# Kernel optimization log

Hardware: AMD Instinct MI355X
Metric: run time of the kernel (lower is better)

Reference implementation:

```python
import jax, jax.numpy as jnp
import numpy as np

B, N, C = 4, 100000, 64
S = 256            # img_size
RADIUS_PX = 1.5    # radius in pixels
K = 8              # points_per_pixel
GAMMA = 1.0
R_NDC = RADIUS_PX / S * 2.0  # radius in NDC, as in forward()


def setup_inputs() -> dict:
    key = jax.random.key(0)
    k1, k2 = jax.random.split(key)
    pts = jax.random.normal(k1, (B, N, 3), dtype=jnp.float32)
    features = jax.random.normal(k2, (B, N, C), dtype=jnp.float32)
    return {"pts": pts, "features": features}


def _rasterize_one(pts_b):
    # pts_b: (N,3) sign-flipped NDC points. Emulates pytorch3d rasterize_points:
    # per pixel keep the K nearest-in-z points whose NDC distance to the pixel
    # center is <= R_NDC (points with z < 0 are culled).
    x, y, z = pts_b[:, 0], pts_b[:, 1], pts_b[:, 2]
    # pytorch3d NDC->pixel: ndc = 1 - 2*(p+0.5)/S  =>  p = (1-ndc)*S/2 - 0.5
    px = (1.0 - x) * (S / 2.0) - 0.5
    py = (1.0 - y) * (S / 2.0) - 0.5
    offs = jnp.arange(-1, 3)  # 4-wide window fully covers a 1.5px radius
    cj = jnp.floor(px).astype(jnp.int32)[:, None] + offs  # (N,4) candidate cols
    ci = jnp.floor(py).astype(jnp.int32)[:, None] + offs  # (N,4) candidate rows
    cx = 1.0 - 2.0 * (cj.astype(pts_b.dtype) + 0.5) / S   # pixel-center NDC x
    cy = 1.0 - 2.0 * (ci.astype(pts_b.dtype) + 0.5) / S   # pixel-center NDC y
    d2 = (cy - y[:, None])[:, :, None] ** 2 + (cx - x[:, None])[:, None, :] ** 2  # (N,4,4)
    pid = ci[:, :, None] * S + cj[:, None, :]                                      # (N,4,4)
    inb = (ci[:, :, None] >= 0) & (ci[:, :, None] < S) & (cj[:, None, :] >= 0) & (cj[:, None, :] < S)
    valid = inb & (d2 <= R_NDC * R_NDC) & (z[:, None, None] >= 0.0)
    pid = jnp.where(valid, pid, S * S).reshape(-1)
    zc = jnp.where(valid, z[:, None, None], jnp.inf).reshape(-1)
    d2f = d2.reshape(-1)
    pidx = jnp.broadcast_to(jnp.arange(N, dtype=jnp.int32)[:, None, None], (N, 4, 4)).reshape(-1)
    order = jnp.lexsort((zc, pid))  # sort by pixel id, then depth (front first)
    pid_s, d2_s, pi_s = pid[order], d2f[order], pidx[order]
    seg_start = jnp.searchsorted(pid_s, pid_s, side='left')
    rank = jnp.arange(pid_s.shape[0]) - seg_start  # per-pixel z-rank
    keep = (pid_s < S * S) & (rank < K)
    pid_w = jnp.where(keep, pid_s, S * S)          # OOB index -> dropped by mode='drop'
    rank_w = jnp.where(keep, rank, 0)
    idx_buf = jnp.full((S * S, K), -1, jnp.int32).at[pid_w, rank_w].set(pi_s, mode='drop')
    d_buf = jnp.zeros((S * S, K), pts_b.dtype).at[pid_w, rank_w].set(d2_s, mode='drop')
    return idx_buf.reshape(S, S, K), d_buf.reshape(S, S, K)


def _forward(pts, features):
    # forward() flips x and y signs in-place
    pts = pts * jnp.array([-1.0, -1.0, 1.0], dtype=pts.dtype)
    idx, d2 = jax.vmap(_rasterize_one)(pts)        # (B,S,S,K) each
    dist = d2 / (R_NDC * R_NDC)
    alphas = 1.0 - jnp.clip(dist, 0.001, 1.0) ** (0.5 * GAMMA)  # .pow(0.5).pow(gamma)
    alphas = jnp.where(idx >= 0, alphas, 0.0)      # alpha_composite skips idx < 0
    trans = jnp.cumprod(1.0 - alphas, axis=-1)     # transmittance, front-to-back
    trans = jnp.concatenate([jnp.ones_like(trans[..., :1]), trans[..., :-1]], axis=-1)
    w = alphas * trans                             # (B,S,S,K) compositing weights
    gath = jax.vmap(lambda f, i: f[jnp.clip(i, 0)])(features, idx)  # (B,S,S,K,C)
    return jnp.einsum('bhwk,bhwkc->bchw', w, gath)  # (B,C,S,S)


def reference(pts, features):
    return _forward(pts, features)
```

## Files before the change

### kernel.cpp

```cpp
#include <hip/hip_runtime.h>
#include <stdint.h>

#pragma clang fp contract(off)

#define S 256
#define NPTS 100000
#define BATCH 4
#define CCH 64
#define K 8
#define CAP 20

static constexpr float R2 = 0.01171875f * 0.01171875f;
static constexpr unsigned long long SENT = 0xFFFFFFFFFFFFFFFFULL;

__global__ __launch_bounds__(256) void scatter_list_kernel(
        const float* __restrict__ pts,
        unsigned int* __restrict__ counts,
        unsigned long long* __restrict__ lists) {
    int gid = blockIdx.x * blockDim.x + threadIdx.x;
    if (gid >= BATCH * NPTS * 16) return;
    int cell = gid & 15;
    int pid  = gid >> 4;
    int b = pid / NPTS;
    int n = pid - b * NPTS;

    const float* p = pts + (size_t)pid * 3;
    float x = -p[0];
    float y = -p[1];
    float z = p[2];
    if (!(z >= 0.0f)) return;

    float px = (1.0f - x) * 128.0f - 0.5f;
    float py = (1.0f - y) * 128.0f - 0.5f;
    int cj0 = (int)floorf(px);
    int ci0 = (int)floorf(py);

    int ci = ci0 - 1 + (cell >> 2);
    int cj = cj0 - 1 + (cell & 3);
    if (ci < 0 || ci >= S || cj < 0 || cj >= S) return;

    float cy = 1.0f - 2.0f * ((float)ci + 0.5f) / 256.0f;
    float cx = 1.0f - 2.0f * ((float)cj + 0.5f) / 256.0f;
    float dy = cy - y;
    float dx = cx - x;
    float d2 = dy * dy + dx * dx;
    if (!(d2 <= R2)) return;

    unsigned long long key =
        ((unsigned long long)__float_as_uint(z) << 32) | (unsigned int)n;
    size_t base = (size_t)b * (S * S) + (size_t)(ci * S + cj);
    unsigned int old = atomicAdd(&counts[base], 1u);
    if (old < CAP) lists[base * CAP + old] = key;
}

#define CSW(a, b) do {                                        \
        unsigned long long _lo = (a) < (b) ? (a) : (b);       \
        unsigned long long _hi = (a) < (b) ? (b) : (a);       \
        (a) = _lo; (b) = _hi;                                 \
    } while (0)
#define INSERT8(x) do {                                       \
        unsigned long long _x = (x);                          \
        t7 = t7 < _x ? t7 : _x;                               \
        CSW(t6, t7); CSW(t5, t6); CSW(t4, t5); CSW(t3, t4);   \
        CSW(t2, t3); CSW(t1, t2); CSW(t0, t1);                \
    } while (0)
#define PAIR(j, q) do {                                                   \
        INSERT8((2 * (j)     < c) ? (q).x : SENT);                        \
        INSERT8((2 * (j) + 1 < c) ? (q).y : SENT);                        \
    } while (0)

__global__ __launch_bounds__(256) void blend_list_kernel(
        const float* __restrict__ pts,
        const float* __restrict__ feat,
        const unsigned int* __restrict__ counts,
        const unsigned long long* __restrict__ lists,
        float* __restrict__ out) {
    int blk = blockIdx.x;
    int logical = (blk & 7) * 512 + (blk >> 3);
    int seg = logical & 3;
    int h   = (logical >> 2) & 255;
    int b   = logical >> 10;
    int tid = threadIdx.x;
    int w0  = seg * 64;

    __shared__ float s_alpha[64][K + 1];
    __shared__ float s_wgt[64][K + 1];
    __shared__ int   s_idx[64][K + 1];
    __shared__ int   s_cnt[64];
    __shared__ unsigned long long s_key[64][K + 1];

    const float* pb = pts + (size_t)b * NPTS * 3;

    if (tid < 64) {
        size_t base = (size_t)b * (S * S) + (size_t)h * S + (size_t)(w0 + tid);
        const ulonglong2* lp2 =
            reinterpret_cast<const ulonglong2*>(lists + base * (size_t)CAP);

        ulonglong2 q0 = lp2[0], q1 = lp2[1], q2 = lp2[2], q3 = lp2[3];
        ulonglong2 q4 = lp2[4], q5 = lp2[5], q6 = lp2[6], q7 = lp2[7];
        ulonglong2 q8 = lp2[8], q9 = lp2[9];
        int c = (int)counts[base];
        if (c > CAP) c = CAP;

        unsigned long long t0 = SENT, t1 = SENT, t2 = SENT, t3 = SENT;
        unsigned long long t4 = SENT, t5 = SENT, t6 = SENT, t7 = SENT;

        PAIR(0, q0); PAIR(1, q1); PAIR(2, q2); PAIR(3, q3); PAIR(4, q4);
        PAIR(5, q5); PAIR(6, q6); PAIR(7, q7); PAIR(8, q8); PAIR(9, q9);

        s_key[tid][0] = t0; s_key[tid][1] = t1;
        s_key[tid][2] = t2; s_key[tid][3] = t3;
        s_key[tid][4] = t4; s_key[tid][5] = t5;
        s_key[tid][6] = t6; s_key[tid][7] = t7;
        s_cnt[tid] = c < K ? c : K;
    }
    __syncthreads();

    for (int e = tid; e < 64 * K; e += 256) {
        int p = e >> 3;
        int k = e & 7;
        unsigned long long key = s_key[p][k];
        float alpha = 0.0f;
        int idx = 0;
        if (key != SENT) {
            idx = (int)(unsigned int)(key & 0xFFFFFFFFULL);
            float x = -pb[(size_t)idx * 3 + 0];
            float y = -pb[(size_t)idx * 3 + 1];
            int w = w0 + p;
            float cy = 1.0f - 2.0f * ((float)h + 0.5f) / 256.0f;
            float cx = 1.0f - 2.0f * ((float)w + 0.5f) / 256.0f;
            float dy = cy - y;
            float dx = cx - x;
            float d2 = dy * dy + dx * dx;
            float dist = d2 / R2;
            dist = fminf(fmaxf(dist, 0.001f), 1.0f);
            alpha = 1.0f - sqrtf(dist);
        }
        s_alpha[p][k] = alpha;
        s_idx[p][k] = idx;
    }
    __syncthreads();

    if (tid < 64) {
        float t = 1.0f;
#pragma unroll
        for (int k = 0; k < K; ++k) {
            float a = s_alpha[tid][k];
            s_wgt[tid][k] = a * t;
            t *= (1.0f - a);
        }
    }
    __syncthreads();

    int wave = tid >> 6;
    int lane = tid & 63;
    int pbase = wave * 16;

    int kmax = 0;
#pragma unroll
    for (int i = 0; i < 16; ++i) {
        int c = s_cnt[pbase + i];
        kmax = c > kmax ? c : kmax;
    }

    float acc[16];
#pragma unroll
    for (int i = 0; i < 16; ++i) acc[i] = 0.0f;

    const float* fbl = feat + (size_t)b * NPTS * CCH + lane;
#pragma unroll 2
    for (int k = 0; k < kmax; ++k) {
        float v[16];
#pragma unroll
        for (int i = 0; i < 16; ++i) {
            int idx = s_idx[pbase + i][k];
            v[i] = fbl[(size_t)idx << 6];
        }
#pragma unroll
        for (int i = 0; i < 16; ++i) {
            acc[i] += s_wgt[pbase + i][k] * v[i];
        }
    }

    size_t obase = (((size_t)b * CCH + lane) * S + h) * S + (size_t)(w0 + pbase);
    float4* o4 = (float4*)(out + obase);
#pragma unroll
    for (int q = 0; q < 4; ++q) {
        o4[q] = make_float4(acc[4 * q + 0], acc[4 * q + 1],
                            acc[4 * q + 2], acc[4 * q + 3]);
    }
}

__global__ __launch_bounds__(256) void scatter_kernel(
        const float* __restrict__ pts,
        unsigned long long* __restrict__ keys) {
    int gid = blockIdx.x * blockDim.x + threadIdx.x;
    if (gid >= BATCH * NPTS * 16) return;
    int cell = gid & 15;
    int pid  = gid >> 4;
    int b = pid / NPTS;
    int n = pid - b * NPTS;

    const float* p = pts + (size_t)pid * 3;
    float x = -p[0];
    float y = -p[1];
    float z = p[2];
    if (!(z >= 0.0f)) return;

    float px = (1.0f - x) * 128.0f - 0.5f;
    float py = (1.0f - y) * 128.0f - 0.5f;
    int cj0 = (int)floorf(px);
    int ci0 = (int)floorf(py);

    int ci = ci0 - 1 + (cell >> 2);
    int cj = cj0 - 1 + (cell & 3);
    if (ci < 0 || ci >= S || cj < 0 || cj >= S) return;

    float cy = 1.0f - 2.0f * ((float)ci + 0.5f) / 256.0f;
    float cx = 1.0f - 2.0f * ((float)cj + 0.5f) / 256.0f;
    float dy = cy - y;
    float dx = cx - x;
    float d2 = dy * dy + dx * dx;
    if (!(d2 <= R2)) return;

    unsigned long long key =
        ((unsigned long long)__float_as_uint(z) << 32) | (unsigned int)n;
    unsigned long long* slot =
        keys + ((size_t)b * S * S + (size_t)(ci * S + cj)) * K;

    if (slot[K - 1] < key) return;

    for (int s = 0; s < K; ++s) {
        if (key == SENT) break;
        unsigned long long old = atomicMin(&slot[s], key);
        key = old > key ? old : key;
    }
}

__global__ __launch_bounds__(256) void blend_kernel(
        const float* __restrict__ pts,
        const float* __restrict__ feat,
        const unsigned long long* __restrict__ keys,
        float* __restrict__ out) {
    int seg = blockIdx.x;
    int h   = blockIdx.y;
    int b   = blockIdx.z;
    int tid = threadIdx.x;
    int w0  = seg * 64;

    __shared__ float s_alpha[64][K + 1];
    __shared__ float s_wgt[64][K + 1];
    __shared__ int   s_idx[64][K + 1];
    __shared__ int   s_cnt[64];

    const unsigned long long* kb =
        keys + ((size_t)b * S * S + (size_t)h * S + w0) * K;
    const float* pb = pts + (size_t)b * NPTS * 3;

    for (int e = tid; e < 64 * K; e += 256) {
        int p = e >> 3;
        int k = e & 7;
        unsigned long long key = kb[(size_t)p * K + k];
        float alpha = 0.0f;
        int idx = -1;
        if (key != SENT) {
            idx = (int)(unsigned int)(key & 0xFFFFFFFFULL);
            float x = -pb[(size_t)idx * 3 + 0];
            float y = -pb[(size_t)idx * 3 + 1];
            int w = w0 + p;
            float cy = 1.0f - 2.0f * ((float)h + 0.5f) / 256.0f;
            float cx = 1.0f - 2.0f * ((float)w + 0.5f) / 256.0f;
            float dy = cy - y;
            float dx = cx - x;
            float d2 = dy * dy + dx * dx;
            float dist = d2 / R2;
            dist = fminf(fmaxf(dist, 0.001f), 1.0f);
            alpha = 1.0f - sqrtf(dist);
        }
        s_alpha[p][k] = alpha;
        s_idx[p][k] = idx;
    }
    __syncthreads();

    if (tid < 64) {
        float t = 1.0f;
        int cnt = 0;
        for (int k = 0; k < K; ++k) {
            int raw = s_idx[tid][k];
            float a = s_alpha[tid][k];
            s_wgt[tid][k] = a * t;
            t *= (1.0f - a);
            if (raw >= 0) cnt = k + 1;
            s_idx[tid][k] = raw < 0 ? 0 : raw;
        }
        s_cnt[tid] = cnt;
    }
    __syncthreads();

    int wave = tid >> 6;
    int lane = tid & 63;
    int pbase = wave * 16;

    int kmax = 0;
#pragma unroll
    for (int i = 0; i < 16; ++i) {
        int c = s_cnt[pbase + i];
        kmax = c > kmax ? c : kmax;
    }

    float acc[16];
#pragma unroll
    for (int i = 0; i < 16; ++i) acc[i] = 0.0f;

    const float* fbl = feat + (size_t)b * NPTS * CCH + lane;
    for (int k = 0; k < kmax; ++k) {
        float v[16];
#pragma unroll
        for (int i = 0; i < 16; ++i) {
            int idx = s_idx[pbase + i][k];
            v[i] = fbl[(size_t)idx << 6];
        }
#pragma unroll
        for (int i = 0; i < 16; ++i) {
            acc[i] += s_wgt[pbase + i][k] * v[i];
        }
    }

    size_t obase = (((size_t)b * CCH + lane) * S + h) * S + (size_t)(w0 + pbase);
    float4* o4 = (float4*)(out + obase);
#pragma unroll
    for (int q = 0; q < 4; ++q) {
        o4[q] = make_float4(acc[4 * q + 0], acc[4 * q + 1],
                            acc[4 * q + 2], acc[4 * q + 3]);
    }
}

extern "C" void kernel_launch(void* const* d_in, const int* in_sizes, int n_in,
                              void* d_out, int out_size, void* d_ws, size_t ws_size,
                              hipStream_t stream) {
    const float* pts  = (const float*)d_in[0];
    const float* feat = (const float*)d_in[1];
    float* out = (float*)d_out;

    size_t cnt_bytes  = (size_t)BATCH * S * S * sizeof(unsigned int);
    size_t list_bytes = (size_t)BATCH * S * S * CAP * sizeof(unsigned long long);
    size_t key_bytes  = (size_t)BATCH * S * S * K * sizeof(unsigned long long);

    if (ws_size >= cnt_bytes + list_bytes) {
        unsigned int* counts = (unsigned int*)d_ws;
        unsigned long long* lists =
            (unsigned long long*)((char*)d_ws + cnt_bytes);
        hipMemsetAsync(counts, 0, cnt_bytes, stream);

        int total = BATCH * NPTS * 16;
        scatter_list_kernel<<<(total + 255) / 256, 256, 0, stream>>>(
            pts, counts, lists);

        blend_list_kernel<<<4096, 256, 0, stream>>>(pts, feat, counts, lists, out);
    } else {
        unsigned long long* keys = (unsigned long long*)d_ws;
        hipMemsetAsync(keys, 0xFF, key_bytes, stream);

        int total = BATCH * NPTS * 16;
        scatter_kernel<<<(total + 255) / 256, 256, 0, stream>>>(pts, keys);

        dim3 grid(S / 64, S, BATCH);
        blend_kernel<<<grid, 256, 0, stream>>>(pts, feat, keys, out);
    }
}
```

Measured before the change: 244.7 us.

## Blend a full image row per block with all threads doing list selection

The blend kernel now processes one full 256-pixel row per block instead of a 64-pixel segment, so all 256 threads run the per-pixel top-K selection rather than only the first 64. The shared key array is dropped in favour of storing indices directly with -1 sentinels, and the weight and transmittance pass is spread over all threads. The feature gather runs four 16-pixel groups per wave. This removes idle threads in the serial phases and cuts the block count fourfold, at the cost of more shared memory per block, fewer blocks, and a longer serial gather loop per wave.

```diff
diff --git a/kernel.cpp b/kernel.cpp
--- a/kernel.cpp
+++ b/kernel.cpp
@@ -69,30 +69,30 @@
         INSERT8((2 * (j) + 1 < c) ? (q).y : SENT);                        \
     } while (0)
 
-__global__ __launch_bounds__(256) void blend_list_kernel(
+__global__ __launch_bounds__(256) void blend_row_kernel(
         const float* __restrict__ pts,
         const float* __restrict__ feat,
         const unsigned int* __restrict__ counts,
         const unsigned long long* __restrict__ lists,
         float* __restrict__ out) {
     int blk = blockIdx.x;
-    int logical = (blk & 7) * 512 + (blk >> 3);
-    int seg = logical & 3;
-    int h   = (logical >> 2) & 255;
-    int b   = logical >> 10;
+    int logical = (blk & 7) * 128 + (blk >> 3);
+    int h   = logical & 255;
+    int b   = logical >> 8;
     int tid = threadIdx.x;
-    int w0  = seg * 64;
-
-    __shared__ float s_alpha[64][K + 1];
-    __shared__ float s_wgt[64][K + 1];
-    __shared__ int   s_idx[64][K + 1];
-    __shared__ int   s_cnt[64];
-    __shared__ unsigned long long s_key[64][K + 1];
+    int wave = tid >> 6;
+    int lane = tid & 63;
+
+    __shared__ float s_alpha[256][K + 1];
+    __shared__ float s_wgt[256][K + 1];
+    __shared__ int   s_idx[256][K + 1];
+    __shared__ int   s_cnt[256];
 
     const float* pb = pts + (size_t)b * NPTS * 3;
 
-    if (tid < 64) {
-        size_t base = (size_t)b * (S * S) + (size_t)h * S + (size_t)(w0 + tid);
+    {
+        int p = wave * 64 + lane;
+        size_t base = (size_t)b * (S * S) + (size_t)h * S + (size_t)p;
         const ulonglong2* lp2 =
             reinterpret_cast<const ulonglong2*>(lists + base * (size_t)CAP);
 
@@ -108,28 +108,29 @@
         PAIR(0, q0); PAIR(1, q1); PAIR(2, q2); PAIR(3, q3); PAIR(4, q4);
         PAIR(5, q5); PAIR(6, q6); PAIR(7, q7); PAIR(8, q8); PAIR(9, q9);
 
-        s_key[tid][0] = t0; s_key[tid][1] = t1;
-        s_key[tid][2] = t2; s_key[tid][3] = t3;
-        s_key[tid][4] = t4; s_key[tid][5] = t5;
-        s_key[tid][6] = t6; s_key[tid][7] = t7;
-        s_cnt[tid] = c < K ? c : K;
-    }
-    __syncthreads();
-
-    for (int e = tid; e < 64 * K; e += 256) {
+        s_idx[p][0] = (t0 == SENT) ? -1 : (int)(unsigned int)t0;
+        s_idx[p][1] = (t1 == SENT) ? -1 : (int)(unsigned int)t1;
+        s_idx[p][2] = (t2 == SENT) ? -1 : (int)(unsigned int)t2;
+        s_idx[p][3] = (t3 == SENT) ? -1 : (int)(unsigned int)t3;
+        s_idx[p][4] = (t4 == SENT) ? -1 : (int)(unsigned int)t4;
+        s_idx[p][5] = (t5 == SENT) ? -1 : (int)(unsigned int)t5;
+        s_idx[p][6] = (t6 == SENT) ? -1 : (int)(unsigned int)t6;
+        s_idx[p][7] = (t7 == SENT) ? -1 : (int)(unsigned int)t7;
+        s_cnt[p] = c < K ? c : K;
+    }
+    __syncthreads();
+
+    float cyr = 1.0f - 2.0f * ((float)h + 0.5f) / 256.0f;
+    for (int e = tid; e < 256 * K; e += 256) {
         int p = e >> 3;
         int k = e & 7;
-        unsigned long long key = s_key[p][k];
+        int idx = s_idx[p][k];
         float alpha = 0.0f;
-        int idx = 0;
-        if (key != SENT) {
-            idx = (int)(unsigned int)(key & 0xFFFFFFFFULL);
+        if (idx >= 0) {
             float x = -pb[(size_t)idx * 3 + 0];
             float y = -pb[(size_t)idx * 3 + 1];
-            int w = w0 + p;
-            float cy = 1.0f - 2.0f * ((float)h + 0.5f) / 256.0f;
-            float cx = 1.0f - 2.0f * ((float)w + 0.5f) / 256.0f;
-            float dy = cy - y;
+            float cx = 1.0f - 2.0f * ((float)p + 0.5f) / 256.0f;
+            float dy = cyr - y;
             float dx = cx - x;
             float d2 = dy * dy + dx * dx;
             float dist = d2 / R2;
@@ -137,57 +138,59 @@
             alpha = 1.0f - sqrtf(dist);
         }
         s_alpha[p][k] = alpha;
-        s_idx[p][k] = idx;
-    }
-    __syncthreads();
-
-    if (tid < 64) {
+    }
+    __syncthreads();
+
+    {
+        int p = tid;
         float t = 1.0f;
 #pragma unroll
         for (int k = 0; k < K; ++k) {
-            float a = s_alpha[tid][k];
-            s_wgt[tid][k] = a * t;
+            float a = s_alpha[p][k];
+            s_wgt[p][k] = a * t;
             t *= (1.0f - a);
-        }
-    }
-    __syncthreads();
-
-    int wave = tid >> 6;
-    int lane = tid & 63;
-    int pbase = wave * 16;
-
-    int kmax = 0;
-#pragma unroll
-    for (int i = 0; i < 16; ++i) {
-        int c = s_cnt[pbase + i];
-        kmax = c > kmax ? c : kmax;
-    }
-
-    float acc[16];
-#pragma unroll
-    for (int i = 0; i < 16; ++i) acc[i] = 0.0f;
+            int raw = s_idx[p][k];
+            s_idx[p][k] = raw < 0 ? 0 : raw;
+        }
+    }
+    __syncthreads();
 
     const float* fbl = feat + (size_t)b * NPTS * CCH + lane;
+    for (int g = 0; g < 4; ++g) {
+        int pbase = wave * 64 + g * 16;
+
+        int kmax = 0;
+#pragma unroll
+        for (int i = 0; i < 16; ++i) {
+            int c = s_cnt[pbase + i];
+            kmax = c > kmax ? c : kmax;
+        }
+
+        float acc[16];
+#pragma unroll
+        for (int i = 0; i < 16; ++i) acc[i] = 0.0f;
+
 #pragma unroll 2
-    for (int k = 0; k < kmax; ++k) {
-        float v[16];
-#pragma unroll
-        for (int i = 0; i < 16; ++i) {
-            int idx = s_idx[pbase + i][k];
-            v[i] = fbl[(size_t)idx << 6];
-        }
-#pragma unroll
-        for (int i = 0; i < 16; ++i) {
-            acc[i] += s_wgt[pbase + i][k] * v[i];
-        }
-    }
-
-    size_t obase = (((size_t)b * CCH + lane) * S + h) * S + (size_t)(w0 + pbase);
-    float4* o4 = (float4*)(out + obase);
-#pragma unroll
-    for (int q = 0; q < 4; ++q) {
-        o4[q] = make_float4(acc[4 * q + 0], acc[4 * q + 1],
-                            acc[4 * q + 2], acc[4 * q + 3]);
+        for (int k = 0; k < kmax; ++k) {
+            float v[16];
+#pragma unroll
+            for (int i = 0; i < 16; ++i) {
+                int idx = s_idx[pbase + i][k];
+                v[i] = fbl[(size_t)idx << 6];
+            }
+#pragma unroll
+            for (int i = 0; i < 16; ++i) {
+                acc[i] += s_wgt[pbase + i][k] * v[i];
+            }
+        }
+
+        size_t obase = (((size_t)b * CCH + lane) * S + h) * S + (size_t)pbase;
+        float4* o4 = (float4*)(out + obase);
+#pragma unroll
+        for (int q = 0; q < 4; ++q) {
+            o4[q] = make_float4(acc[4 * q + 0], acc[4 * q + 1],
+                                acc[4 * q + 2], acc[4 * q + 3]);
+        }
     }
 }
 
@@ -356,7 +359,8 @@
         scatter_list_kernel<<<(total + 255) / 256, 256, 0, stream>>>(
             pts, counts, lists);
 
-        blend_list_kernel<<<4096, 256, 0, stream>>>(pts, feat, counts, lists, out);
+        blend_row_kernel<<<BATCH * S, 256, 0, stream>>>(
+            pts, feat, counts, lists, out);
     } else {
         unsigned long long* keys = (unsigned long long*)d_ws;
         hipMemsetAsync(keys, 0xFF, key_bytes, stream);
```

Result: slower. 257.9 us (+5.4%).

## Precompute alpha in scatter and carry it through per-pixel top-K selection

Applied to the files above, without the earlier changes.

The scatter kernel now computes each point's alpha for its target pixel and stores it in a parallel float list next to the depth/index keys. The blend kernel sorts key/alpha pairs together, computes compositing weights directly in registers, and drops the second pass that re-gathered point coordinates and recomputed distances, removing two barriers and a random global read. In exchange, scatter writes an extra 4 bytes per candidate, blend reads an extra 80 bytes per pixel, and the sorting network moves twice the data. The fast path also now requires a larger workspace; if it is not available, execution falls back to the slower path.

```diff
diff --git a/kernel.cpp b/kernel.cpp
--- a/kernel.cpp
+++ b/kernel.cpp
@@ -16,7 +16,8 @@
 __global__ __launch_bounds__(256) void scatter_list_kernel(
         const float* __restrict__ pts,
         unsigned int* __restrict__ counts,
-        unsigned long long* __restrict__ lists) {
+        unsigned long long* __restrict__ lists,
+        float* __restrict__ lists_a) {
     int gid = blockIdx.x * blockDim.x + threadIdx.x;
     if (gid >= BATCH * NPTS * 16) return;
     int cell = gid & 15;
@@ -46,34 +47,44 @@
     float d2 = dy * dy + dx * dx;
     if (!(d2 <= R2)) return;
 
+    float dist = d2 / R2;
+    dist = fminf(fmaxf(dist, 0.001f), 1.0f);
+    float alpha = 1.0f - sqrtf(dist);
+
     unsigned long long key =
         ((unsigned long long)__float_as_uint(z) << 32) | (unsigned int)n;
     size_t base = (size_t)b * (S * S) + (size_t)(ci * S + cj);
     unsigned int old = atomicAdd(&counts[base], 1u);
-    if (old < CAP) lists[base * CAP + old] = key;
-}
-
-#define CSW(a, b) do {                                        \
-        unsigned long long _lo = (a) < (b) ? (a) : (b);       \
-        unsigned long long _hi = (a) < (b) ? (b) : (a);       \
-        (a) = _lo; (b) = _hi;                                 \
+    if (old < CAP) {
+        lists[base * CAP + old] = key;
+        lists_a[base * CAP + old] = alpha;
+    }
+}
+
+#define CSWP(ka, aa, kb, ab) do {                             \
+        bool _lt = (ka) < (kb);                               \
+        unsigned long long _kl = _lt ? (ka) : (kb);           \
+        unsigned long long _kh = _lt ? (kb) : (ka);           \
+        float _al = _lt ? (aa) : (ab);                        \
+        float _ah = _lt ? (ab) : (aa);                        \
+        (ka) = _kl; (kb) = _kh; (aa) = _al; (ab) = _ah;       \
     } while (0)
-#define INSERT8(x) do {                                       \
-        unsigned long long _x = (x);                          \
-        t7 = t7 < _x ? t7 : _x;                               \
-        CSW(t6, t7); CSW(t5, t6); CSW(t4, t5); CSW(t3, t4);   \
-        CSW(t2, t3); CSW(t1, t2); CSW(t0, t1);                \
+#define INS8P(e, kk, aa) do {                                             \
+        unsigned long long _k = ((e) < c) ? (kk) : SENT;                  \
+        float _a = ((e) < c) ? (aa) : 0.0f;                               \
+        bool _r = _k < t7;                                                \
+        t7 = _r ? _k : t7; a7 = _r ? _a : a7;                             \
+        CSWP(t6, a6, t7, a7); CSWP(t5, a5, t6, a6);                       \
+        CSWP(t4, a4, t5, a5); CSWP(t3, a3, t4, a4);                       \
+        CSWP(t2, a2, t3, a3); CSWP(t1, a1, t2, a2);                       \
+        CSWP(t0, a0, t1, a1);                                             \
     } while (0)
-#define PAIR(j, q) do {                                                   \
-        INSERT8((2 * (j)     < c) ? (q).x : SENT);                        \
-        INSERT8((2 * (j) + 1 < c) ? (q).y : SENT);                        \
-    } while (0)
 
 __global__ __launch_bounds__(256) void blend_list_kernel(
-        const float* __restrict__ pts,
         const float* __restrict__ feat,
         const unsigned int* __restrict__ counts,
         const unsigned long long* __restrict__ lists,
+        const float* __restrict__ lists_a,
         float* __restrict__ out) {
     int blk = blockIdx.x;
     int logical = (blk & 7) * 512 + (blk >> 3);
@@ -83,72 +94,58 @@
     int tid = threadIdx.x;
     int w0  = seg * 64;
 
-    __shared__ float s_alpha[64][K + 1];
     __shared__ float s_wgt[64][K + 1];
     __shared__ int   s_idx[64][K + 1];
     __shared__ int   s_cnt[64];
-    __shared__ unsigned long long s_key[64][K + 1];
-
-    const float* pb = pts + (size_t)b * NPTS * 3;
 
     if (tid < 64) {
         size_t base = (size_t)b * (S * S) + (size_t)h * S + (size_t)(w0 + tid);
         const ulonglong2* lp2 =
             reinterpret_cast<const ulonglong2*>(lists + base * (size_t)CAP);
+        const float4* ap4 =
+            reinterpret_cast<const float4*>(lists_a + base * (size_t)CAP);
 
         ulonglong2 q0 = lp2[0], q1 = lp2[1], q2 = lp2[2], q3 = lp2[3];
         ulonglong2 q4 = lp2[4], q5 = lp2[5], q6 = lp2[6], q7 = lp2[7];
         ulonglong2 q8 = lp2[8], q9 = lp2[9];
+        float4 f0 = ap4[0], f1 = ap4[1], f2 = ap4[2], f3 = ap4[3], f4 = ap4[4];
         int c = (int)counts[base];
         if (c > CAP) c = CAP;
 
         unsigned long long t0 = SENT, t1 = SENT, t2 = SENT, t3 = SENT;
         unsigned long long t4 = SENT, t5 = SENT, t6 = SENT, t7 = SENT;
-
-        PAIR(0, q0); PAIR(1, q1); PAIR(2, q2); PAIR(3, q3); PAIR(4, q4);
-        PAIR(5, q5); PAIR(6, q6); PAIR(7, q7); PAIR(8, q8); PAIR(9, q9);
-
-        s_key[tid][0] = t0; s_key[tid][1] = t1;
-        s_key[tid][2] = t2; s_key[tid][3] = t3;
-        s_key[tid][4] = t4; s_key[tid][5] = t5;
-        s_key[tid][6] = t6; s_key[tid][7] = t7;
+        float a0 = 0.0f, a1 = 0.0f, a2 = 0.0f, a3 = 0.0f;
+        float a4 = 0.0f, a5 = 0.0f, a6 = 0.0f, a7 = 0.0f;
+
+        INS8P(0,  q0.x, f0.x); INS8P(1,  q0.y, f0.y);
+        INS8P(2,  q1.x, f0.z); INS8P(3,  q1.y, f0.w);
+        INS8P(4,  q2.x, f1.x); INS8P(5,  q2.y, f1.y);
+        INS8P(6,  q3.x, f1.z); INS8P(7,  q3.y, f1.w);
+        INS8P(8,  q4.x, f2.x); INS8P(9,  q4.y, f2.y);
+        INS8P(10, q5.x, f2.z); INS8P(11, q5.y, f2.w);
+        INS8P(12, q6.x, f3.x); INS8P(13, q6.y, f3.y);
+        INS8P(14, q7.x, f3.z); INS8P(15, q7.y, f3.w);
+        INS8P(16, q8.x, f4.x); INS8P(17, q8.y, f4.y);
+        INS8P(18, q9.x, f4.z); INS8P(19, q9.y, f4.w);
+
+        float t = 1.0f;
+        s_wgt[tid][0] = a0 * t; t *= (1.0f - a0);
+        s_wgt[tid][1] = a1 * t; t *= (1.0f - a1);
+        s_wgt[tid][2] = a2 * t; t *= (1.0f - a2);
+        s_wgt[tid][3] = a3 * t; t *= (1.0f - a3);
+        s_wgt[tid][4] = a4 * t; t *= (1.0f - a4);
+        s_wgt[tid][5] = a5 * t; t *= (1.0f - a5);
+        s_wgt[tid][6] = a6 * t; t *= (1.0f - a6);
+        s_wgt[tid][7] = a7 * t;
+        s_idx[tid][0] = (t0 == SENT) ? 0 : (int)(unsigned int)t0;
+        s_idx[tid][1] = (t1 == SENT) ? 0 : (int)(unsigned int)t1;
+        s_idx[tid][2] = (t2 == SENT) ? 0 : (int)(unsigned int)t2;
+        s_idx[tid][3] = (t3 == SENT) ? 0 : (int)(unsigned int)t3;
+        s_idx[tid][4] = (t4 == SENT) ? 0 : (int)(unsigned int)t4;
+        s_idx[tid][5] = (t5 == SENT) ? 0 : (int)(unsigned int)t5;
+        s_idx[tid][6] = (t6 == SENT) ? 0 : (int)(unsigned int)t6;
+        s_idx[tid][7] = (t7 == SENT) ? 0 : (int)(unsigned int)t7;
         s_cnt[tid] = c < K ? c : K;
-    }
-    __syncthreads();
-
-    for (int e = tid; e < 64 * K; e += 256) {
-        int p = e >> 3;
-        int k = e & 7;
-        unsigned long long key = s_key[p][k];
-        float alpha = 0.0f;
-        int idx = 0;
-        if (key != SENT) {
-            idx = (int)(unsigned int)(key & 0xFFFFFFFFULL);
-            float x = -pb[(size_t)idx * 3 + 0];
-            float y = -pb[(size_t)idx * 3 + 1];
-            int w = w0 + p;
-            float cy = 1.0f - 2.0f * ((float)h + 0.5f) / 256.0f;
-            float cx = 1.0f - 2.0f * ((float)w + 0.5f) / 256.0f;
-            float dy = cy - y;
-            float dx = cx - x;
-            float d2 = dy * dy + dx * dx;
-            float dist = d2 / R2;
-            dist = fminf(fmaxf(dist, 0.001f), 1.0f);
-            alpha = 1.0f - sqrtf(dist);
-        }
-        s_alpha[p][k] = alpha;
-        s_idx[p][k] = idx;
-    }
-    __syncthreads();
-
-    if (tid < 64) {
-        float t = 1.0f;
-#pragma unroll
-        for (int k = 0; k < K; ++k) {
-            float a = s_alpha[tid][k];
-            s_wgt[tid][k] = a * t;
-            t *= (1.0f - a);
-        }
     }
     __syncthreads();
 
@@ -344,19 +341,22 @@
 
     size_t cnt_bytes  = (size_t)BATCH * S * S * sizeof(unsigned int);
     size_t list_bytes = (size_t)BATCH * S * S * CAP * sizeof(unsigned long long);
+    size_t alpha_bytes = (size_t)BATCH * S * S * CAP * sizeof(float);
     size_t key_bytes  = (size_t)BATCH * S * S * K * sizeof(unsigned long long);
 
-    if (ws_size >= cnt_bytes + list_bytes) {
+    if (ws_size >= cnt_bytes + list_bytes + alpha_bytes) {
         unsigned int* counts = (unsigned int*)d_ws;
         unsigned long long* lists =
             (unsigned long long*)((char*)d_ws + cnt_bytes);
+        float* lists_a = (float*)((char*)d_ws + cnt_bytes + list_bytes);
         hipMemsetAsync(counts, 0, cnt_bytes, stream);
 
         int total = BATCH * NPTS * 16;
         scatter_list_kernel<<<(total + 255) / 256, 256, 0, stream>>>(
-            pts, counts, lists);
-
-        blend_list_kernel<<<4096, 256, 0, stream>>>(pts, feat, counts, lists, out);
+            pts, counts, lists, lists_a);
+
+        blend_list_kernel<<<4096, 256, 0, stream>>>(
+            feat, counts, lists, lists_a, out);
     } else {
         unsigned long long* keys = (unsigned long long*)d_ws;
         hipMemsetAsync(keys, 0xFF, key_bytes, stream);
```

Measured after the change: 252.0 us. 3.0% more time.
